# Optimization experiments

Measured on AMD Instinct MI355X. Metric: run time of the kernel, lower is better.

## Reference

```python
import jax, jax.numpy as jnp
import numpy as np

NUM_HEADS = 16
HIDDEN = 1024
HEAD_DIM = HIDDEN // NUM_HEADS
B, S, D = 2, 2048, 1024


def setup_inputs() -> dict:
    key = jax.random.key(0)
    ks = jax.random.split(key, 7)
    scale = 1.0 / np.sqrt(D)
    return {
        "query": jax.random.normal(ks[0], (B, S, D), dtype=jnp.float32),
        "key": jax.random.normal(ks[1], (B, S, D), dtype=jnp.float32),
        "value": jax.random.normal(ks[2], (B, S, D), dtype=jnp.float32),
        "Wk_w": jax.random.normal(ks[3], (HIDDEN, D), dtype=jnp.float32) * scale,
        "Wk_b": jax.random.normal(ks[4], (HIDDEN,), dtype=jnp.float32) * scale,
        "Wv_w": jax.random.normal(ks[5], (HIDDEN, D), dtype=jnp.float32) * scale,
        "Wv_b": jax.random.normal(ks[6], (HIDDEN,), dtype=jnp.float32) * scale,
    }


def reference(query, key, value, Wk_w, Wk_b, Wv_w, Wv_b):
    # NOTE: in the original torch module, self.W_v is assigned twice, so the
    # SAME Linear (Wv) projects both key and value; Wk projects query.
    b, s, _ = query.shape

    def split_heads(x):  # [b,s,hidden] -> [b,h,s,hd]
        return x.reshape(b, s, NUM_HEADS, HEAD_DIM).transpose(0, 2, 1, 3)

    q = split_heads(query @ Wk_w.T + Wk_b)
    k = split_heads(key @ Wv_w.T + Wv_b)
    v = split_heads(value @ Wv_w.T + Wv_b)

    scores = jnp.einsum("bhqd,bhkd->bhqk", q, k) / jnp.sqrt(
        jnp.asarray(HEAD_DIM, dtype=q.dtype))
    probs = jax.nn.softmax(scores, axis=-1)
    out = jnp.einsum("bhqk,bhkd->bhqd", probs, v)
    return out.transpose(0, 2, 1, 3).reshape(b, s, NUM_HEADS * HEAD_DIM)
```

## Files before the change

### kernel.cpp

```cpp
#include <hip/hip_runtime.h>
#include <stdint.h>

typedef unsigned short u16;
typedef uint32_t u32;
typedef __bf16 bf16x8 __attribute__((ext_vector_type(8)));
typedef float f32x4 __attribute__((ext_vector_type(4)));
typedef float f32x16 __attribute__((ext_vector_type(16)));
typedef u16 u16x4 __attribute__((ext_vector_type(4)));
typedef u16 u16x8 __attribute__((ext_vector_type(8)));

#define XQ_OFF 0ul
#define XK_OFF 4194304ul
#define XV_OFF 8388608ul
#define WK_OFF 12582912ul
#define WV_OFF 13631488ul
#define Q_OFF  14680064ul
#define K_OFF  18874368ul
#define V_OFF  23068672ul

#define SCQ 0.18033688011112042f

#if __has_builtin(__builtin_amdgcn_exp2f)
#define EXP2F(x) __builtin_amdgcn_exp2f(x)
#else
#define EXP2F(x) exp2f(x)
#endif

__device__ __forceinline__ u16 f2bf(float f) {
  u32 u = __float_as_uint(f);
  u32 r = (u + 0x7fffu + ((u >> 16) & 1u)) >> 16;
  return (u16)r;
}

__device__ __forceinline__ u32 pk2(float a, float b) {
  typedef __bf16 bf2_t __attribute__((ext_vector_type(2)));
  typedef float f2_t __attribute__((ext_vector_type(2)));
  f2_t v; v[0] = a; v[1] = b;
  bf2_t h = __builtin_convertvector(v, bf2_t);
  union { bf2_t h; u32 u; } cv; cv.h = h; return cv.u;
}

__device__ __forceinline__ void load_lds16(const void* g, void* l) {
  __builtin_amdgcn_global_load_lds(
      (const __attribute__((address_space(1))) u32*)g,
      (__attribute__((address_space(3))) u32*)l, 16, 0, 0);
}

__global__ __launch_bounds__(256) void cvt_tile_kernel(
    const float* __restrict__ xq, const float* __restrict__ xk,
    const float* __restrict__ xv, const float* __restrict__ wk,
    const float* __restrict__ wv, u16* __restrict__ ws) {
  __shared__ u16 tile[4096];
  const int bid = blockIdx.x;
  const float* src; size_t dstbase; int rt, ktp;
  if (bid < 3072) {
    int m = bid >> 10, loc = bid & 1023;
    src = (m == 0) ? xq : (m == 1) ? xk : xv;
    dstbase = (size_t)m * 4194304ul;
    rt = loc >> 4; ktp = loc & 15;
  } else {
    int r2 = bid - 3072;
    int m = r2 >> 8, loc = r2 & 255;
    src = m ? wv : wk;
    dstbase = WK_OFF + (size_t)m * 1048576ul;
    rt = loc >> 4; ktp = loc & 15;
  }
  const int t = threadIdx.x;
  const int row0 = t >> 4, c = t & 15;
  const int k = c * 4;
  const float* s = src + (size_t)(rt * 64 + row0) * 1024ul + ktp * 64 + k;
#pragma unroll
  for (int i = 0; i < 4; ++i) {
    float4 v = *(const float4*)(s + (size_t)i * 16384ul);
    int row = row0 + i * 16;
    u32* p = (u32*)(tile + ((k >> 5) * 2048 + ((k >> 3) & 3) * 512 + row * 8 + (k & 7)));
    p[0] = pk2(v.x, v.y);
    p[1] = pk2(v.z, v.w);
  }
  __syncthreads();
  u16* dst = ws + dstbase + (size_t)(rt * 32 + ktp * 2) * 2048ul;
#pragma unroll
  for (int so = 0; so < 4096; so += 2048)
    *(u16x8*)(dst + so + t * 8) = *(const u16x8*)(tile + so + t * 8);
}

__global__ __launch_bounds__(256, 3) void proj_kernel(u16* __restrict__ ws,
                                                      const float* __restrict__ bk,
                                                      const float* __restrict__ bv) {
  const int proj = blockIdx.z;
  const int mtile = blockIdx.x;
  const int ntile = blockIdx.y;
  const u16* A = ws + (size_t)proj * 4194304ul;
  const u16* Bw = ws + ((proj == 0) ? WK_OFF : WV_OFF);
  const float* bias = (proj == 0) ? bk : bv;
  u16* outQ = ws + Q_OFF;
  u16* outK = ws + K_OFF;
  u16* outV = ws + V_OFF;

  const int t = threadIdx.x;
  const int w = t >> 6, lane = t & 63;
  const int wm = w >> 1, wn = w & 1;
  const int c32 = lane & 31, g2 = lane >> 5;

  const u16* Aw = A + (size_t)(2 * mtile + wm) * 65536ul + (size_t)g2 * 512ul + (size_t)c32 * 8ul;
  const u16* Bb = Bw + (size_t)(2 * ntile + wn) * 65536ul + (size_t)g2 * 512ul + (size_t)c32 * 8ul;

  f32x16 acc[2][2];
#pragma unroll
  for (int rf = 0; rf < 2; ++rf)
#pragma unroll
    for (int cf = 0; cf < 2; ++cf)
#pragma unroll
      for (int i = 0; i < 16; ++i) acc[rf][cf][i] = 0.f;

  bf16x8 ab[4][2], bb[4][2];
#pragma unroll
  for (int s = 0; s < 4; ++s)
#pragma unroll
    for (int f = 0; f < 2; ++f) {
      ab[s][f] = *(const bf16x8*)(Aw + (size_t)s * 1024ul + f * 256);
      bb[s][f] = *(const bf16x8*)(Bb + (size_t)s * 1024ul + f * 256);
    }

#pragma unroll 1
  for (int ks = 0; ks < 60; ks += 4) {
#pragma unroll
    for (int s = 0; s < 4; ++s) {
#pragma unroll
      for (int rf = 0; rf < 2; ++rf)
#pragma unroll
        for (int cf = 0; cf < 2; ++cf)
          acc[rf][cf] =
              __builtin_amdgcn_mfma_f32_32x32x16_bf16(ab[s][rf], bb[s][cf], acc[rf][cf], 0, 0, 0);
      const size_t o = (size_t)(ks + 4 + s) * 1024ul;
#pragma unroll
      for (int f = 0; f < 2; ++f) {
        ab[s][f] = *(const bf16x8*)(Aw + o + f * 256);
        bb[s][f] = *(const bf16x8*)(Bb + o + f * 256);
      }
    }
  }
#pragma unroll
  for (int s = 0; s < 4; ++s)
#pragma unroll
    for (int rf = 0; rf < 2; ++rf)
#pragma unroll
      for (int cf = 0; cf < 2; ++cf)
        acc[rf][cf] =
            __builtin_amdgcn_mfma_f32_32x32x16_bf16(ab[s][rf], bb[s][cf], acc[rf][cf], 0, 0, 0);

  const int m0w = mtile * 128 + wm * 64, n0w = ntile * 128 + wn * 64;
#pragma unroll
  for (int cf = 0; cf < 2; ++cf) {
    const int col = n0w + cf * 32 + c32;
    const float bvv = bias[col];
    const int h = col >> 6, d = col & 63;
#pragma unroll
    for (int rf = 0; rf < 2; ++rf) {
#pragma unroll
      for (int q = 0; q < 4; ++q) {
        const int mbase = m0w + rf * 32 + q * 8 + g2 * 4;
        const int b = mbase >> 11;
        const int bh = b * 16 + h;
        if (proj == 2) {
          const int s = mbase & 2047;
          u16x4 pk;
#pragma unroll
          for (int r = 0; r < 4; ++r) pk[r] = f2bf(acc[rf][cf][q * 4 + r] + bvv);
          size_t idx = (size_t)bh * 131072ul + (size_t)(s >> 6) * 4096ul +
                       (size_t)((s & 63) >> 3) * 512ul + (size_t)d * 8ul + (size_t)(s & 7);
          *(u16x4*)(outV + idx) = pk;
        } else {
          u16* dst = (proj == 0) ? outQ : outK;
#pragma unroll
          for (int r = 0; r < 4; ++r) {
            const int m = mbase + r;
            const int s = m & 2047;
            float y = acc[rf][cf][q * 4 + r] + bvv;
            if (proj == 0) y *= SCQ;
            size_t idx;
            if (proj == 0)
              idx = (size_t)bh * 131072ul + (size_t)(s >> 7) * 8192ul + (size_t)(d >> 3) * 1024ul +
                    (size_t)(s & 127) * 8ul + (size_t)(d & 7);
            else
              idx = (size_t)bh * 131072ul + (size_t)(s >> 6) * 4096ul + (size_t)(d >> 3) * 512ul +
                    (size_t)(s & 63) * 8ul + (size_t)(d & 7);
            dst[idx] = f2bf(y);
          }
        }
      }
    }
  }
}

__global__ __launch_bounds__(512, 4) void attn_kernel(const u16* __restrict__ ws,
                                                      float* __restrict__ out) {
  const int bh = blockIdx.x, qtile = blockIdx.y;
  const int b = bh >> 4, h = bh & 15;
  const int t = threadIdx.x, w = t >> 6, lane = t & 63, g = lane >> 4, c = lane & 15;

  __shared__ u16 Ks[2][4096];
  __shared__ u16 Vs[2][4096];
  __shared__ __align__(16) u16 Ps[8][640];

  const u16* Qg = ws + Q_OFF + (size_t)bh * 131072ul + (size_t)qtile * 8192ul;
  const u16* Kg = ws + K_OFF + (size_t)bh * 131072ul;
  const u16* Vg = ws + V_OFF + (size_t)bh * 131072ul;

  const int off = t * 16;
  load_lds16((const char*)Kg + off, (char*)Ks[0] + off);
  load_lds16((const char*)Vg + off, (char*)Vs[0] + off);

  bf16x8 qf[2];
#pragma unroll
  for (int ks = 0; ks < 2; ++ks)
    qf[ks] = *(const bf16x8*)(Qg + (ks * 4 + g) * 1024 + (w * 16 + c) * 8);

  u16x8 ou;
#pragma unroll
  for (int i = 0; i < 8; ++i) ou[i] = (u16)0x3F80;
  union { u16x8 u; bf16x8 b; } ocv; ocv.u = ou;
  const bf16x8 onesf = ocv.b;

  f32x4 O[4], Lacc;
  Lacc = (f32x4){0.f, 0.f, 0.f, 0.f};
#pragma unroll
  for (int nt = 0; nt < 4; ++nt) O[nt] = (f32x4){0.f, 0.f, 0.f, 0.f};

  u16* Psw = Ps[w];
  __syncthreads();

#pragma unroll 1
  for (int j = 0; j < 32; ++j) {
    const int cur = j & 1;
    if (j < 31) {
      const char* Kn = (const char*)(Kg + (size_t)(j + 1) * 4096ul);
      const char* Vn = (const char*)(Vg + (size_t)(j + 1) * 4096ul);
      load_lds16(Kn + off, (char*)Ks[cur ^ 1] + off);
      load_lds16(Vn + off, (char*)Vs[cur ^ 1] + off);
    }
    const u16* Kc = Ks[cur];
    const u16* Vc = Vs[cur];

    f32x4 St[4];
#pragma unroll
    for (int mtk = 0; mtk < 4; ++mtk) St[mtk] = (f32x4){0.f, 0.f, 0.f, 0.f};
#pragma unroll
    for (int ks = 0; ks < 2; ++ks) {
      bf16x8 kf[4];
#pragma unroll
      for (int mtk = 0; mtk < 4; ++mtk)
        kf[mtk] = *(const bf16x8*)(Kc + (ks * 4 + g) * 512 + (mtk * 16 + c) * 8);
#pragma unroll
      for (int mtk = 0; mtk < 4; ++mtk)
        St[mtk] = __builtin_amdgcn_mfma_f32_16x16x32_bf16(kf[mtk], qf[ks], St[mtk], 0, 0, 0);
    }
#pragma unroll
    for (int mtk = 0; mtk < 4; ++mtk)
#pragma unroll
      for (int r = 0; r < 4; ++r) St[mtk][r] = EXP2F(St[mtk][r]);
#pragma unroll
    for (int ksh = 0; ksh < 2; ++ksh) {
#pragma unroll
      for (int m2 = 0; m2 < 2; ++m2) {
        const int mtk = ksh * 2 + m2;
        u32 lo = pk2(St[mtk][0], St[mtk][1]);
        u32 hi = pk2(St[mtk][2], St[mtk][3]);
        u32* p = (u32*)(Psw + c * 40 + m2 * 16 + g * 4);
        p[0] = lo; p[1] = hi;
      }
      asm volatile("s_waitcnt lgkmcnt(0)" ::: "memory");
      bf16x8 pf, vf[4];
      pf = *(const bf16x8*)(Psw + c * 40 + g * 8);
#pragma unroll
      for (int nt = 0; nt < 4; ++nt)
        vf[nt] = *(const bf16x8*)(Vc + (ksh * 4 + g) * 512 + (nt * 16 + c) * 8);
      Lacc = __builtin_amdgcn_mfma_f32_16x16x32_bf16(pf, onesf, Lacc, 0, 0, 0);
#pragma unroll
      for (int nt = 0; nt < 4; ++nt)
        O[nt] = __builtin_amdgcn_mfma_f32_16x16x32_bf16(pf, vf[nt], O[nt], 0, 0, 0);
    }
    __syncthreads();
  }

  const int q0 = qtile * 128 + w * 16;
#pragma unroll
  for (int r = 0; r < 4; ++r) {
    const float inv = 1.0f / Lacc[r];
    const int q = q0 + g * 4 + r;
    float* rowp = out + (size_t)(b * 2048 + q) * 1024ul + h * 64;
#pragma unroll
    for (int nt = 0; nt < 4; ++nt) rowp[nt * 16 + c] = O[nt][r] * inv;
  }
}

extern "C" void kernel_launch(void* const* d_in, const int* in_sizes, int n_in,
                              void* d_out, int out_size, void* d_ws, size_t ws_size,
                              hipStream_t stream) {
  const float* q = (const float*)d_in[0];
  const float* k = (const float*)d_in[1];
  const float* v = (const float*)d_in[2];
  const float* wk = (const float*)d_in[3];
  const float* bk = (const float*)d_in[4];
  const float* wv = (const float*)d_in[5];
  const float* bv = (const float*)d_in[6];
  u16* ws = (u16*)d_ws;
  float* out = (float*)d_out;

  cvt_tile_kernel<<<3584, 256, 0, stream>>>(q, k, v, wk, wv, ws);
  proj_kernel<<<dim3(32, 8, 3), 256, 0, stream>>>(ws, bk, bv);
  attn_kernel<<<dim3(32, 16), 512, 0, stream>>>(ws, out);
}
```

Measured before the change: 184.8 us.

## Drop LDS K/V staging, load fragments from global with 32-row waves

Rewrites the attention kernel so that K and V fragments are read straight from global memory into registers, replacing the double-buffered LDS tiles. The K fragment for the next block is prefetched while the current block is processed. Each wave now handles 32 query rows instead of 16, so the block shrinks to 256 threads and every K/V fragment feeds twice as many MFMAs. This removes the per-iteration __syncthreads and the LDS traffic for K/V. In exchange it raises register pressure and relies on L2/L1 to absorb the repeated global reads across waves.

```diff
diff --git a/kernel.cpp b/kernel.cpp
--- a/kernel.cpp
+++ b/kernel.cpp
@@ -193,28 +193,24 @@
   }
 }
 
-__global__ __launch_bounds__(512, 4) void attn_kernel(const u16* __restrict__ ws,
+__global__ __launch_bounds__(256, 2) void attn_kernel(const u16* __restrict__ ws,
                                                       float* __restrict__ out) {
   const int bh = blockIdx.x, qtile = blockIdx.y;
   const int b = bh >> 4, h = bh & 15;
   const int t = threadIdx.x, w = t >> 6, lane = t & 63, g = lane >> 4, c = lane & 15;
 
-  __shared__ u16 Ks[2][4096];
-  __shared__ u16 Vs[2][4096];
-  __shared__ __align__(16) u16 Ps[8][640];
+  __shared__ __align__(16) u16 Ps[4][1280];
 
   const u16* Qg = ws + Q_OFF + (size_t)bh * 131072ul + (size_t)qtile * 8192ul;
   const u16* Kg = ws + K_OFF + (size_t)bh * 131072ul;
   const u16* Vg = ws + V_OFF + (size_t)bh * 131072ul;
 
-  const int off = t * 16;
-  load_lds16((const char*)Kg + off, (char*)Ks[0] + off);
-  load_lds16((const char*)Vg + off, (char*)Vs[0] + off);
-
-  bf16x8 qf[2];
-#pragma unroll
-  for (int ks = 0; ks < 2; ++ks)
-    qf[ks] = *(const bf16x8*)(Qg + (ks * 4 + g) * 1024 + (w * 16 + c) * 8);
+  bf16x8 qf[2][2];
+#pragma unroll
+  for (int ntq = 0; ntq < 2; ++ntq)
+#pragma unroll
+    for (int ks = 0; ks < 2; ++ks)
+      qf[ntq][ks] = *(const bf16x8*)(Qg + (ks * 4 + g) * 1024 + (w * 32 + ntq * 16 + c) * 8);
 
   u16x8 ou;
 #pragma unroll
@@ -222,76 +218,100 @@
   union { u16x8 u; bf16x8 b; } ocv; ocv.u = ou;
   const bf16x8 onesf = ocv.b;
 
-  f32x4 O[4], Lacc;
-  Lacc = (f32x4){0.f, 0.f, 0.f, 0.f};
-#pragma unroll
-  for (int nt = 0; nt < 4; ++nt) O[nt] = (f32x4){0.f, 0.f, 0.f, 0.f};
+  f32x4 O[2][4], Lacc[2];
+#pragma unroll
+  for (int mtq = 0; mtq < 2; ++mtq) {
+    Lacc[mtq] = (f32x4){0.f, 0.f, 0.f, 0.f};
+#pragma unroll
+    for (int nt = 0; nt < 4; ++nt) O[mtq][nt] = (f32x4){0.f, 0.f, 0.f, 0.f};
+  }
 
   u16* Psw = Ps[w];
-  __syncthreads();
+
+  bf16x8 kf[2][4];
+#pragma unroll
+  for (int ks = 0; ks < 2; ++ks)
+#pragma unroll
+    for (int mtk = 0; mtk < 4; ++mtk)
+      kf[ks][mtk] = *(const bf16x8*)(Kg + (ks * 4 + g) * 512 + (mtk * 16 + c) * 8);
 
 #pragma unroll 1
   for (int j = 0; j < 32; ++j) {
-    const int cur = j & 1;
-    if (j < 31) {
-      const char* Kn = (const char*)(Kg + (size_t)(j + 1) * 4096ul);
-      const char* Vn = (const char*)(Vg + (size_t)(j + 1) * 4096ul);
-      load_lds16(Kn + off, (char*)Ks[cur ^ 1] + off);
-      load_lds16(Vn + off, (char*)Vs[cur ^ 1] + off);
-    }
-    const u16* Kc = Ks[cur];
-    const u16* Vc = Vs[cur];
-
-    f32x4 St[4];
-#pragma unroll
-    for (int mtk = 0; mtk < 4; ++mtk) St[mtk] = (f32x4){0.f, 0.f, 0.f, 0.f};
-#pragma unroll
-    for (int ks = 0; ks < 2; ++ks) {
-      bf16x8 kf[4];
+    const u16* Vj = Vg + (size_t)j * 4096ul;
+    bf16x8 vf[2][4];
+#pragma unroll
+    for (int ksh = 0; ksh < 2; ++ksh)
+#pragma unroll
+      for (int nt = 0; nt < 4; ++nt)
+        vf[ksh][nt] = *(const bf16x8*)(Vj + (ksh * 4 + g) * 512 + (nt * 16 + c) * 8);
+
+    f32x4 St[4][2];
+#pragma unroll
+    for (int mtk = 0; mtk < 4; ++mtk)
+#pragma unroll
+      for (int ntq = 0; ntq < 2; ++ntq) St[mtk][ntq] = (f32x4){0.f, 0.f, 0.f, 0.f};
+#pragma unroll
+    for (int ks = 0; ks < 2; ++ks)
 #pragma unroll
       for (int mtk = 0; mtk < 4; ++mtk)
-        kf[mtk] = *(const bf16x8*)(Kc + (ks * 4 + g) * 512 + (mtk * 16 + c) * 8);
+#pragma unroll
+        for (int ntq = 0; ntq < 2; ++ntq)
+          St[mtk][ntq] =
+              __builtin_amdgcn_mfma_f32_16x16x32_bf16(kf[ks][mtk], qf[ntq][ks], St[mtk][ntq], 0, 0, 0);
+
+    const u16* Kn = Kg + (size_t)((j < 31) ? (j + 1) : 31) * 4096ul;
+#pragma unroll
+    for (int ks = 0; ks < 2; ++ks)
 #pragma unroll
       for (int mtk = 0; mtk < 4; ++mtk)
-        St[mtk] = __builtin_amdgcn_mfma_f32_16x16x32_bf16(kf[mtk], qf[ks], St[mtk], 0, 0, 0);
-    }
+        kf[ks][mtk] = *(const bf16x8*)(Kn + (ks * 4 + g) * 512 + (mtk * 16 + c) * 8);
+
 #pragma unroll
     for (int mtk = 0; mtk < 4; ++mtk)
 #pragma unroll
-      for (int r = 0; r < 4; ++r) St[mtk][r] = EXP2F(St[mtk][r]);
+      for (int ntq = 0; ntq < 2; ++ntq)
+#pragma unroll
+        for (int r = 0; r < 4; ++r) St[mtk][ntq][r] = EXP2F(St[mtk][ntq][r]);
+
 #pragma unroll
     for (int ksh = 0; ksh < 2; ++ksh) {
 #pragma unroll
-      for (int m2 = 0; m2 < 2; ++m2) {
-        const int mtk = ksh * 2 + m2;
-        u32 lo = pk2(St[mtk][0], St[mtk][1]);
-        u32 hi = pk2(St[mtk][2], St[mtk][3]);
-        u32* p = (u32*)(Psw + c * 40 + m2 * 16 + g * 4);
-        p[0] = lo; p[1] = hi;
+      for (int ntq = 0; ntq < 2; ++ntq)
+#pragma unroll
+        for (int m2 = 0; m2 < 2; ++m2) {
+          const int mtk = ksh * 2 + m2;
+          u32 lo = pk2(St[mtk][ntq][0], St[mtk][ntq][1]);
+          u32 hi = pk2(St[mtk][ntq][2], St[mtk][ntq][3]);
+          u32* p = (u32*)(Psw + (ntq * 16 + c) * 40 + m2 * 16 + g * 4);
+          p[0] = lo; p[1] = hi;
+        }
+      asm volatile("s_waitcnt lgkmcnt(0)" ::: "memory");
+      bf16x8 pf[2];
+#pragma unroll
+      for (int mtq = 0; mtq < 2; ++mtq)
+        pf[mtq] = *(const bf16x8*)(Psw + (mtq * 16 + c) * 40 + g * 8);
+#pragma unroll
+      for (int mtq = 0; mtq < 2; ++mtq) {
+        Lacc[mtq] = __builtin_amdgcn_mfma_f32_16x16x32_bf16(pf[mtq], onesf, Lacc[mtq], 0, 0, 0);
+#pragma unroll
+        for (int nt = 0; nt < 4; ++nt)
+          O[mtq][nt] =
+              __builtin_amdgcn_mfma_f32_16x16x32_bf16(pf[mtq], vf[ksh][nt], O[mtq][nt], 0, 0, 0);
       }
-      asm volatile("s_waitcnt lgkmcnt(0)" ::: "memory");
-      bf16x8 pf, vf[4];
-      pf = *(const bf16x8*)(Psw + c * 40 + g * 8);
-#pragma unroll
-      for (int nt = 0; nt < 4; ++nt)
-        vf[nt] = *(const bf16x8*)(Vc + (ksh * 4 + g) * 512 + (nt * 16 + c) * 8);
-      Lacc = __builtin_amdgcn_mfma_f32_16x16x32_bf16(pf, onesf, Lacc, 0, 0, 0);
-#pragma unroll
-      for (int nt = 0; nt < 4; ++nt)
-        O[nt] = __builtin_amdgcn_mfma_f32_16x16x32_bf16(pf, vf[nt], O[nt], 0, 0, 0);
-    }
-    __syncthreads();
-  }
-
-  const int q0 = qtile * 128 + w * 16;
-#pragma unroll
-  for (int r = 0; r < 4; ++r) {
-    const float inv = 1.0f / Lacc[r];
-    const int q = q0 + g * 4 + r;
-    float* rowp = out + (size_t)(b * 2048 + q) * 1024ul + h * 64;
-#pragma unroll
-    for (int nt = 0; nt < 4; ++nt) rowp[nt * 16 + c] = O[nt][r] * inv;
-  }
+    }
+  }
+
+  const int q0 = qtile * 128 + w * 32;
+#pragma unroll
+  for (int mtq = 0; mtq < 2; ++mtq)
+#pragma unroll
+    for (int r = 0; r < 4; ++r) {
+      const float inv = 1.0f / Lacc[mtq][r];
+      const int q = q0 + mtq * 16 + g * 4 + r;
+      float* rowp = out + (size_t)(b * 2048 + q) * 1024ul + h * 64;
+#pragma unroll
+      for (int nt = 0; nt < 4; ++nt) rowp[nt * 16 + c] = O[mtq][nt][r] * inv;
+    }
 }
 
 extern "C" void kernel_launch(void* const* d_in, const int* in_sizes, int n_in,
@@ -309,5 +329,5 @@
 
   cvt_tile_kernel<<<3584, 256, 0, stream>>>(q, k, v, wk, wv, ws);
   proj_kernel<<<dim3(32, 8, 3), 256, 0, stream>>>(ws, bk, bv);
-  attn_kernel<<<dim3(32, 16), 512, 0, stream>>>(ws, out);
-}
+  attn_kernel<<<dim3(32, 16), 256, 0, stream>>>(ws, out);
+}
```

Measured after the change: 183.1 us. About the same (-0.9%).
